# Performance work log

Measured on AMD Instinct MI355X. Metric: run time of the kernel, lower is better.

## Reference

```python
import jax, jax.numpy as jnp
import numpy as np

jax.config.update("jax_enable_x64", True)  # original casts to double for Sinkhorn

SINKHORN_EPS = 0.003
SINKHORN_ITER = 50
MU = 0.25


def setup_inputs() -> dict:
    key = jax.random.key(0)
    k1, k2 = jax.random.split(key)
    x = jax.random.normal(k1, (4096, 4096), dtype=jnp.float32)        # [B, D]
    codebook = jax.random.normal(k2, (256, 4096), dtype=jnp.float32)  # [K, D]
    return {"x": x, "codebook": codebook}


def _sinkhorn_probs(d2term):
    # d2term: [B, K] squared distances (float32)
    B, K = d2term.shape
    max_d = jnp.max(d2term, axis=-1, keepdims=True)
    min_d = jnp.min(d2term, axis=-1, keepdims=True)
    mid_d = (max_d + min_d) / 2
    normed = ((d2term - mid_d) / (max_d - mid_d + 1e-8)).astype(jnp.float64)
    standard = jnp.exp(-normed / SINKHORN_EPS)
    standard = standard / standard.sum()  # sum over dim1 then dim0 == total sum

    def body(i, carry):
        s, n = carry
        s = s / s.sum(axis=0, keepdims=True)
        n = n / K
        s = s / s.sum(axis=1, keepdims=True)
        n = n / B
        return (s, n)

    standard, normed = jax.lax.fori_loop(0, SINKHORN_ITER, body, (standard, normed))
    # original returns d2term_normed * B as probs (d2term_standard is unused after loop)
    return normed * B


def reference(x, codebook):
    # squared euclidean distances: [B, K]
    d2term = (jnp.sum(x * x, axis=-1, keepdims=True)
              + jnp.sum(codebook * codebook, axis=-1)[None, :]
              - 2.0 * (x @ codebook.T))
    probs = _sinkhorn_probs(d2term)              # [B, K] float64
    indices = jnp.argmax(probs, axis=-1)         # [B] int
    quant_hard = codebook[indices]               # [B, D] gather
    # straight-through estimator
    quant = jax.lax.stop_gradient(quant_hard - x) + x
    codebook_loss = jnp.mean((quant_hard - jax.lax.stop_gradient(x)) ** 2, axis=-1)
    commitment_loss = jnp.mean((jax.lax.stop_gradient(quant_hard) - x) ** 2, axis=-1)
    loss = codebook_loss + MU * commitment_loss  # [B]
    return quant, indices, probs, loss
```

## Files before the change

kernel.cpp:

```cpp
#include <hip/hip_runtime.h>
#include <hip/hip_bf16.h>
#include <math.h>

#define D_DIM   4096
#define B_ROWS  4096
#define K_CODES 256
#define MARGIN  3.0
#define BK      128
#define NITER   (D_DIM / BK)
#define MT      16

#define IDX_OFF   (B_ROWS * D_DIM)
#define PROBS_OFF (IDX_OFF + B_ROWS)
#define LOSS_OFF  (PROBS_OFF + B_ROWS * K_CODES)

typedef __bf16 bf16x8 __attribute__((ext_vector_type(8)));
typedef float  f32x4  __attribute__((ext_vector_type(4)));


static __device__ inline unsigned short f2bf(float f) {
    __hip_bfloat16 h = __float2bfloat16(f);
    return *reinterpret_cast<unsigned short*>(&h);
}

__global__ __launch_bounds__(64) void prep_cb(const float* __restrict__ cb,
                                              unsigned short* __restrict__ cbsw,
                                              double* __restrict__ cc) {
    const int lane = threadIdx.x & 63;
    const int k = blockIdx.x;
    const float4* row4 = (const float4*)(cb + (size_t)k * D_DIM);
    double a0 = 0.0, a1 = 0.0, a2 = 0.0, a3 = 0.0;
#pragma unroll
    for (int i = 0; i < 16; ++i) {
        float4 v = row4[i * 64 + lane];
        a0 += (double)v.x * v.x; a1 += (double)v.y * v.y;
        a2 += (double)v.z * v.z; a3 += (double)v.w * v.w;
        ushort4 h;
        h.x = f2bf(v.x); h.y = f2bf(v.y); h.z = f2bf(v.z); h.w = f2bf(v.w);
        const int c = (i * 64 + lane) * 4;
        const size_t idx = (((size_t)(c >> 5) * 16 + (k >> 4)) * 64
                            + ((c >> 3) & 3) * 16 + (k & 15)) * 8 + (c & 7);
        *(ushort4*)&cbsw[idx] = h;
    }
    double s = (a0 + a1) + (a2 + a3);
    for (int off = 32; off; off >>= 1) s += __shfl_xor(s, off);
    if (lane == 0) cc[k] = s;
}

#define LOAD_BANK(bank, Lbase)                                              \
    _Pragma("unroll")                                                       \
    for (int s = 0; s < 4; ++s) {                                           \
        bank[s][0] = *(const bf16x8*)(bbase + ((size_t)(Lbase) + s) * 8192);        \
        bank[s][1] = *(const bf16x8*)(bbase + ((size_t)(Lbase) + s) * 8192 + 512);  \
    }

#define MFMA_TILE(Ap, bank)                                                 \
    _Pragma("unroll")                                                       \
    for (int s = 0; s < 4; ++s) {                                           \
        bf16x8 af = *(const bf16x8*)&Ap[(s * 64 + lane) * 8];               \
        acc0 = __builtin_amdgcn_mfma_f32_16x16x32_bf16(af, bank[s][0], acc0, 0, 0, 0); \
        acc1 = __builtin_amdgcn_mfma_f32_16x16x32_bf16(af, bank[s][1], acc1, 0, 0, 0); \
    }

#define STAGE_A(buf, v)                                                     \
    {                                                                       \
        ushort4 hh;                                                         \
        hh.x = f2bf((v).x); hh.y = f2bf((v).y);                             \
        hh.z = f2bf((v).z); hh.w = f2bf((v).w);                             \
        *(ushort4*)&buf[aw] = hh;                                           \
        sq += (v).x*(v).x + (v).y*(v).y + (v).z*(v).z + (v).w*(v).w;        \
    }

__global__ __launch_bounds__(512, 2) void vq(const float* __restrict__ x,
                                             const float* __restrict__ cb,
                                             const unsigned short* __restrict__ cbsw,
                                             const double* __restrict__ cc,
                                             float* __restrict__ out) {
    __shared__ unsigned short As[2][2048];
    __shared__ float d2s[MT][K_CODES];
    __shared__ float xxs[MT];
    const int t = threadIdx.x;
    const int lane = t & 63, w = t >> 6;
    const int m0 = blockIdx.x * MT;

    const int arow = t >> 5;
    const int ak = (t & 31) * 4;
    const float* ag = x + (size_t)(m0 + arow) * D_DIM + ak;
    const int aw = (ak >> 3) * 128 + arow * 8 + (ak & 7);
    const unsigned short* bbase = cbsw + ((size_t)w * 128 + lane) * 8;

    f32x4 acc0 = {0.f, 0.f, 0.f, 0.f}, acc1 = {0.f, 0.f, 0.f, 0.f};
    float sq = 0.f;

    bf16x8 bA[4][2], bB[4][2];

    LOAD_BANK(bA, 0)
    float4 p0 = *(const float4*)(ag);
    float4 cA = *(const float4*)(ag + BK);
    float4 cB;
    STAGE_A(As[0], p0)
    asm volatile("s_waitcnt lgkmcnt(0)" ::: "memory");
    __builtin_amdgcn_s_barrier();
    __builtin_amdgcn_sched_barrier(0);

    for (int itp = 0; itp < 16; ++itp) {
        STAGE_A(As[1], cA)
        {
            const int nt = (2 * itp + 2 < NITER) ? (2 * itp + 2) : 0;
            cB = *(const float4*)(ag + (size_t)nt * BK);
        }
        LOAD_BANK(bB, (2 * itp + 1) * 4)
        __builtin_amdgcn_s_setprio(1);
        MFMA_TILE(As[0], bA)
        __builtin_amdgcn_s_setprio(0);
        asm volatile("s_waitcnt lgkmcnt(0)" ::: "memory");
        __builtin_amdgcn_s_barrier();
        __builtin_amdgcn_sched_barrier(0);

        if (itp < 15) STAGE_A(As[0], cB)
        {
            const int nt = (2 * itp + 3 < NITER) ? (2 * itp + 3) : 0;
            cA = *(const float4*)(ag + (size_t)nt * BK);
        }
        {
            const int Lb = (2 * itp + 2 < NITER) ? (2 * itp + 2) * 4 : 0;
            LOAD_BANK(bA, Lb)
        }
        __builtin_amdgcn_s_setprio(1);
        MFMA_TILE(As[1], bB)
        __builtin_amdgcn_s_setprio(0);
        asm volatile("s_waitcnt lgkmcnt(0)" ::: "memory");
        __builtin_amdgcn_s_barrier();
        __builtin_amdgcn_sched_barrier(0);
    }

#pragma unroll
    for (int r = 0; r < 4; ++r) {
        const int orow = (lane >> 4) * 4 + r;
        d2s[orow][w * 32 + (lane & 15)]      = acc0[r];
        d2s[orow][w * 32 + 16 + (lane & 15)] = acc1[r];
    }
    sq += __shfl_xor(sq, 1); sq += __shfl_xor(sq, 2); sq += __shfl_xor(sq, 4);
    sq += __shfl_xor(sq, 8); sq += __shfl_xor(sq, 16);
    if ((t & 31) == 0) xxs[arow] = sq;
    __syncthreads();

#pragma unroll
    for (int rr = 0; rr < 2; ++rr) {
        const int r = w + 8 * rr;
        const int row = m0 + r;
        const double xx = (double)xxs[r];
        const float4 dv = ((const float4*)&d2s[r][0])[lane];
        double v[4];
        v[0] = xx + cc[4 * lane + 0] - 2.0 * (double)dv.x;
        v[1] = xx + cc[4 * lane + 1] - 2.0 * (double)dv.y;
        v[2] = xx + cc[4 * lane + 2] - 2.0 * (double)dv.z;
        v[3] = xx + cc[4 * lane + 3] - 2.0 * (double)dv.w;

        double mx = fmax(fmax(v[0], v[1]), fmax(v[2], v[3]));
        for (int off = 32; off; off >>= 1) mx = fmax(mx, __shfl_xor(mx, off));
        const double thr = mx - MARGIN;

        unsigned long long b[4];
#pragma unroll
        for (int j = 0; j < 4; ++j) b[j] = __ballot(v[j] >= thr);
        const int total = __popcll(b[0]) + __popcll(b[1]) + __popcll(b[2]) + __popcll(b[3]);

        int bestk = 0; double best;
        if (total == 1) {
            best = mx;
#pragma unroll
            for (int j = 0; j < 4; ++j)
                if (b[j]) bestk = 4 * (int)__builtin_ctzll(b[j]) + j;
        } else {
            const float4* xrow4 = (const float4*)(x + (size_t)row * D_DIM);
            int flags = 0;
#pragma unroll
            for (int j = 0; j < 4; ++j) if (v[j] >= thr) flags |= 1 << j;
            unsigned long long cand = __ballot(flags != 0);
            best = -1.0e300;
            while (cand) {
                const int lsrc = __builtin_ctzll(cand);
                cand &= cand - 1;
                const int f = __shfl(flags, lsrc);
                for (int j = 0; j < 4; ++j) {
                    if (!((f >> j) & 1)) continue;
                    const int k = 4 * lsrc + j;
                    const float4* crow4 = (const float4*)(cb + (size_t)k * D_DIM);
                    double a0 = 0.0, a1 = 0.0, a2 = 0.0, a3 = 0.0;
#pragma unroll
                    for (int i = 0; i < 16; ++i) {
                        float4 xa = xrow4[i * 64 + lane];
                        float4 ca = crow4[i * 64 + lane];
                        a0 += (double)xa.x * ca.x; a1 += (double)xa.y * ca.y;
                        a2 += (double)xa.z * ca.z; a3 += (double)xa.w * ca.w;
                    }
                    double s = (a0 + a1) + (a2 + a3);
                    for (int off = 32; off; off >>= 1) s += __shfl_xor(s, off);
                    const double d2e = xx + cc[k] - 2.0 * s;
                    if (d2e > best) { best = d2e; bestk = k; }
                }
            }
        }

        if (lane == 0) {
            out[IDX_OFF + row]  = (float)bestk;
            out[LOSS_OFF + row] = (float)(1.25 * best / (double)D_DIM);
        }
        float4 z = make_float4(0.f, 0.f, 0.f, 0.f);
        ((float4*)(out + PROBS_OFF + (size_t)row * K_CODES))[lane] = z;
        const float4* src = (const float4*)(cb + (size_t)bestk * D_DIM);
        float4* dst = (float4*)(out + (size_t)row * D_DIM);
#pragma unroll
        for (int i = 0; i < 16; ++i) dst[i * 64 + lane] = src[i * 64 + lane];
    }
}

extern "C" void kernel_launch(void* const* d_in, const int* in_sizes, int n_in,
                              void* d_out, int out_size, void* d_ws, size_t ws_size,
                              hipStream_t stream) {
    const float* x  = (const float*)d_in[0];
    const float* cb = (const float*)d_in[1];
    float* out = (float*)d_out;

    unsigned short* cbsw = (unsigned short*)d_ws;
    double*         cc   = (double*)((char*)d_ws + (size_t)K_CODES * D_DIM * sizeof(unsigned short));

    hipLaunchKernelGGL(prep_cb, dim3(256), dim3(64),  0, stream, cb, cbsw, cc);
    hipLaunchKernelGGL(vq,      dim3(256), dim3(512), 0, stream, x, cb, cbsw, cc, out);
}
```

Baseline: 157.4 us.

## Stage codebook tiles into LDS via async global_load_lds triple buffer

Each block now loads codebook tiles straight into shared memory with global_load_lds, using a three-deep ring buffer instead of per-wave register prefetch banks. The K step drops from 128 to 64 so the tiles fit, and a vmcnt-based wait keeps one or two tiles in flight. The goal is to hide codebook load latency and free the registers that held the prefetch banks. In exchange, LDS use rises to about 96KB per block, the two-blocks-per-CU launch bound is removed, and there are twice as many barriers along the K loop.

```diff
diff --git a/kernel.cpp b/kernel.cpp
--- a/kernel.cpp
+++ b/kernel.cpp
@@ -6,7 +6,7 @@
 #define B_ROWS  4096
 #define K_CODES 256
 #define MARGIN  3.0
-#define BK      128
+#define BK      64
 #define NITER   (D_DIM / BK)
 #define MT      16
 
@@ -47,36 +47,13 @@
     if (lane == 0) cc[k] = s;
 }
 
-#define LOAD_BANK(bank, Lbase)                                              \
-    _Pragma("unroll")                                                       \
-    for (int s = 0; s < 4; ++s) {                                           \
-        bank[s][0] = *(const bf16x8*)(bbase + ((size_t)(Lbase) + s) * 8192);        \
-        bank[s][1] = *(const bf16x8*)(bbase + ((size_t)(Lbase) + s) * 8192 + 512);  \
-    }
-
-#define MFMA_TILE(Ap, bank)                                                 \
-    _Pragma("unroll")                                                       \
-    for (int s = 0; s < 4; ++s) {                                           \
-        bf16x8 af = *(const bf16x8*)&Ap[(s * 64 + lane) * 8];               \
-        acc0 = __builtin_amdgcn_mfma_f32_16x16x32_bf16(af, bank[s][0], acc0, 0, 0, 0); \
-        acc1 = __builtin_amdgcn_mfma_f32_16x16x32_bf16(af, bank[s][1], acc1, 0, 0, 0); \
-    }
-
-#define STAGE_A(buf, v)                                                     \
-    {                                                                       \
-        ushort4 hh;                                                         \
-        hh.x = f2bf((v).x); hh.y = f2bf((v).y);                             \
-        hh.z = f2bf((v).z); hh.w = f2bf((v).w);                             \
-        *(ushort4*)&buf[aw] = hh;                                           \
-        sq += (v).x*(v).x + (v).y*(v).y + (v).z*(v).z + (v).w*(v).w;        \
-    }
-
-__global__ __launch_bounds__(512, 2) void vq(const float* __restrict__ x,
-                                             const float* __restrict__ cb,
-                                             const unsigned short* __restrict__ cbsw,
-                                             const double* __restrict__ cc,
-                                             float* __restrict__ out) {
-    __shared__ unsigned short As[2][2048];
+__global__ __launch_bounds__(512) void vq(const float* __restrict__ x,
+                                          const float* __restrict__ cb,
+                                          const unsigned short* __restrict__ cbsw,
+                                          const double* __restrict__ cc,
+                                          float* __restrict__ out) {
+    __shared__ unsigned short Bs[3][16384];
+    __shared__ unsigned short As[2][1024];
     __shared__ float d2s[MT][K_CODES];
     __shared__ float xxs[MT];
     const int t = threadIdx.x;
@@ -84,54 +61,75 @@
     const int m0 = blockIdx.x * MT;
 
     const int arow = t >> 5;
-    const int ak = (t & 31) * 4;
-    const float* ag = x + (size_t)(m0 + arow) * D_DIM + ak;
+    const int ak = (t & 31) * 2;
+    const float2* ag2 = (const float2*)(x + (size_t)(m0 + arow) * D_DIM + ak);
     const int aw = (ak >> 3) * 128 + arow * 8 + (ak & 7);
-    const unsigned short* bbase = cbsw + ((size_t)w * 128 + lane) * 8;
+    const int brd = w * 1024 + lane * 8;
 
     f32x4 acc0 = {0.f, 0.f, 0.f, 0.f}, acc1 = {0.f, 0.f, 0.f, 0.f};
     float sq = 0.f;
 
-    bf16x8 bA[4][2], bB[4][2];
-
-    LOAD_BANK(bA, 0)
-    float4 p0 = *(const float4*)(ag);
-    float4 cA = *(const float4*)(ag + BK);
-    float4 cB;
-    STAGE_A(As[0], p0)
-    asm volatile("s_waitcnt lgkmcnt(0)" ::: "memory");
+#pragma unroll
+    for (int r = 0; r < 4; ++r)
+        __builtin_amdgcn_global_load_lds(
+            (const __attribute__((address_space(1))) void*)(cbsw + r * 4096 + t * 8),
+            (__attribute__((address_space(3))) void*)(&Bs[0][r * 4096 + t * 8]),
+            16, 0, 0);
+#pragma unroll
+    for (int r = 0; r < 4; ++r)
+        __builtin_amdgcn_global_load_lds(
+            (const __attribute__((address_space(1))) void*)(cbsw + 16384 + r * 4096 + t * 8),
+            (__attribute__((address_space(3))) void*)(&Bs[1][r * 4096 + t * 8]),
+            16, 0, 0);
+    float2 a0v   = ag2[0];
+    float2 cprev = ag2[32];
+    {
+        ushort2 hh; hh.x = f2bf(a0v.x); hh.y = f2bf(a0v.y);
+        *(ushort2*)&As[0][aw] = hh;
+        sq += a0v.x * a0v.x + a0v.y * a0v.y;
+    }
+    asm volatile("s_waitcnt vmcnt(1) lgkmcnt(0)" ::: "memory");
     __builtin_amdgcn_s_barrier();
     __builtin_amdgcn_sched_barrier(0);
 
-    for (int itp = 0; itp < 16; ++itp) {
-        STAGE_A(As[1], cA)
-        {
-            const int nt = (2 * itp + 2 < NITER) ? (2 * itp + 2) : 0;
-            cB = *(const float4*)(ag + (size_t)nt * BK);
-        }
-        LOAD_BANK(bB, (2 * itp + 1) * 4)
+    int bp_r = 0;
+    for (int kt = 0; kt < NITER; ++kt) {
+        const int p = kt & 1;
+        const int bp_w = (bp_r >= 1) ? bp_r - 1 : 2;
+
+        const int ktB = (kt + 2 < NITER) ? kt + 2 : 0;
+        const unsigned short* src = cbsw + (size_t)ktB * 16384 + t * 8;
+#pragma unroll
+        for (int r = 0; r < 4; ++r)
+            __builtin_amdgcn_global_load_lds(
+                (const __attribute__((address_space(1))) void*)(src + r * 4096),
+                (__attribute__((address_space(3))) void*)(&Bs[bp_w][r * 4096 + t * 8]),
+                16, 0, 0);
+        const int ktA = (kt + 2 < NITER) ? kt + 2 : 0;
+        float2 cnew = ag2[(size_t)ktA * 32];
+
         __builtin_amdgcn_s_setprio(1);
-        MFMA_TILE(As[0], bA)
+#pragma unroll
+        for (int s = 0; s < 2; ++s) {
+            bf16x8 af = *(const bf16x8*)&As[p][(s * 64 + lane) * 8];
+            bf16x8 b0 = *(const bf16x8*)&Bs[bp_r][s * 8192 + brd];
+            bf16x8 b1 = *(const bf16x8*)&Bs[bp_r][s * 8192 + brd + 512];
+            acc0 = __builtin_amdgcn_mfma_f32_16x16x32_bf16(af, b0, acc0, 0, 0, 0);
+            acc1 = __builtin_amdgcn_mfma_f32_16x16x32_bf16(af, b1, acc1, 0, 0, 0);
+        }
         __builtin_amdgcn_s_setprio(0);
-        asm volatile("s_waitcnt lgkmcnt(0)" ::: "memory");
+
+        if (kt + 1 < NITER) {
+            ushort2 hh; hh.x = f2bf(cprev.x); hh.y = f2bf(cprev.y);
+            *(ushort2*)&As[p ^ 1][aw] = hh;
+            sq += cprev.x * cprev.x + cprev.y * cprev.y;
+        }
+
+        asm volatile("s_waitcnt vmcnt(5) lgkmcnt(0)" ::: "memory");
         __builtin_amdgcn_s_barrier();
         __builtin_amdgcn_sched_barrier(0);
-
-        if (itp < 15) STAGE_A(As[0], cB)
-        {
-            const int nt = (2 * itp + 3 < NITER) ? (2 * itp + 3) : 0;
-            cA = *(const float4*)(ag + (size_t)nt * BK);
-        }
-        {
-            const int Lb = (2 * itp + 2 < NITER) ? (2 * itp + 2) * 4 : 0;
-            LOAD_BANK(bA, Lb)
-        }
-        __builtin_amdgcn_s_setprio(1);
-        MFMA_TILE(As[1], bB)
-        __builtin_amdgcn_s_setprio(0);
-        asm volatile("s_waitcnt lgkmcnt(0)" ::: "memory");
-        __builtin_amdgcn_s_barrier();
-        __builtin_amdgcn_sched_barrier(0);
+        cprev = cnew;
+        bp_r = (bp_r < 2) ? bp_r + 1 : 0;
     }
 
 #pragma unroll
```

Result: slower. 186.5 us (+18.5%).
